# Kernel tuning notes

Hardware: AMD Instinct MI355X
Metric: run time of the kernel (lower is better)

The kernel has to match this reference:

```python
import jax, jax.numpy as jnp
import numpy as np

B, S, D, H, MLP = 8, 1024, 768, 12, 3072
HD = D // H
EPS = 1e-5


def setup_inputs() -> dict:
    key = jax.random.key(0)
    ks = jax.random.split(key, 5)
    sd = lambda fan_in: 1.0 / np.sqrt(fan_in)
    return {
        "x": jax.random.normal(ks[0], (B, S, D), jnp.float32),
        "w_qkv": jax.random.normal(ks[1], (D, 3 * D), jnp.float32) * sd(D),
        "w_out": jax.random.normal(ks[2], (D, D), jnp.float32) * sd(D),
        "b_out": jnp.zeros((D,), jnp.float32),
        "w1": jax.random.normal(ks[3], (D, MLP), jnp.float32) * sd(D),
        "b1": jnp.zeros((MLP,), jnp.float32),
        "w2": jax.random.normal(ks[4], (MLP, D), jnp.float32) * sd(MLP),
        "b2": jnp.zeros((D,), jnp.float32),
    }


def _instance_norm(x):
    # torch InstanceNorm2d on a 3D [B,S,D] tensor treats it as unbatched (C,H,W):
    # normalize over (S, D) per batch element, biased var, eps=1e-5, no affine.
    mu = jnp.mean(x, axis=(1, 2), keepdims=True)
    var = jnp.mean(jnp.square(x - mu), axis=(1, 2), keepdims=True)
    return (x - mu) * jax.lax.rsqrt(var + EPS)


def reference(x, w_qkv, w_out, b_out, w1, b1, w2, b2):
    scale = HD ** -0.5
    # --- self-attention branch ---
    h = _instance_norm(x)
    qkv = (h @ w_qkv).reshape(B, S, 3, H, HD)          # (qkv, heads, head_dim) split
    qkv = qkv.transpose(2, 0, 3, 1, 4)                  # [3, B, H, S, HD]
    q, k, v = qkv[0], qkv[1], qkv[2]
    att = jax.nn.softmax(jnp.einsum('bhxd,bhyd->bhxy', q, k) * scale, axis=-1)
    o = jnp.einsum('bhxy,bhyd->bhxd', att, v)           # [B, H, S, HD]
    o = o.transpose(0, 2, 1, 3).reshape(B, S, D)        # b h l d -> b l (h d)
    x = x + (o @ w_out + b_out)
    # --- MLP branch (exact erf GELU, as nn.GELU default) ---
    h2 = _instance_norm(x)
    m = jax.nn.gelu(h2 @ w1 + b1, approximate=False) @ w2 + b2
    return x + m
```

## Files before the change

kernel.cpp:

```cpp
#include <hip/hip_runtime.h>
#include <hip/hip_bf16.h>

typedef __hip_bfloat16 bf16;
typedef __attribute__((ext_vector_type(8))) short short8;
typedef __attribute__((ext_vector_type(4))) float f32x4;

#define B_   8
#define S_   1024
#define D_   768
#define H_   12
#define HD_  64
#define MLP_ 3072
#define SD_  (S_ * D_)

#define QSCALE 0.18033688011112042f

__device__ __forceinline__ float b2f(short h) {
  union { unsigned u; float f; } w;
  w.u = ((unsigned)(unsigned short)h) << 16;
  return w.f;
}

__device__ __forceinline__ float fast_exp2(float x) {
  float r;
  asm("v_exp_f32 %0, %1" : "=v"(r) : "v"(x));
  return r;
}

__device__ __forceinline__ bf16 fastbf(float f) {
  union { float f; unsigned u; } w; w.f = f;
  unsigned r = (w.u + 0x7FFF + ((w.u >> 16) & 1)) >> 16;
  union { unsigned short s; bf16 b; } o; o.s = (unsigned short)r;
  return o.b;
}

__device__ __forceinline__ float roundbf(float f) {
  union { float f; unsigned u; } w; w.f = f;
  w.u = ((w.u + 0x7FFF + ((w.u >> 16) & 1)) >> 16) << 16;
  return w.f;
}

__device__ __forceinline__ void gl2lds16(const bf16* g, bf16* l) {
  __builtin_amdgcn_global_load_lds(
      (const __attribute__((address_space(1))) unsigned*)(const void*)g,
      (__attribute__((address_space(3))) unsigned*)(void*)l, 16, 0, 0);
}

__global__ __launch_bounds__(256) void transpose_stats(
    const float* __restrict__ w_qkv, const float* __restrict__ w_out,
    const float* __restrict__ w1, const float* __restrict__ w2,
    bf16* __restrict__ t_qkv, bf16* __restrict__ t_out,
    bf16* __restrict__ t1, bf16* __restrict__ t2,
    const float* __restrict__ x, bf16* __restrict__ xb,
    float* __restrict__ redp, float* __restrict__ cs1, float* __restrict__ csq,
    float* __restrict__ red2) {
  const int t = blockIdx.x;
  if (t == 0 && threadIdx.x < 16) red2[threadIdx.x] = 0.f;

  if (t >= 7680) {
    const float* wsrc; float* cdst; int C, n0;
    if (t < 7692) { wsrc = w1;    cdst = cs1; C = 3072; n0 = (t - 7680) * 256; }
    else          { wsrc = w_qkv; cdst = csq; C = 2304; n0 = (t - 7692) * 256; }
    const int n = n0 + threadIdx.x;
    float s = 0.f;
#pragma unroll 8
    for (int k = 0; k < 768; ++k)
      s += roundbf(wsrc[(long)k * C + n]);
    cdst[n] = s;
    return;
  }

  if (t >= 6912) {
    const int bi = t - 6912;
    const long off = (long)bi * 8192;
    float s = 0.f, s2 = 0.f;
#pragma unroll
    for (int it = 0; it < 4; ++it) {
      const long i = off + ((long)threadIdx.x + it * 256) * 8;
      float4 v0 = *(const float4*)(x + i);
      float4 v1 = *(const float4*)(x + i + 4);
      s += v0.x + v0.y + v0.z + v0.w + v1.x + v1.y + v1.z + v1.w;
      s2 += v0.x * v0.x + v0.y * v0.y + v0.z * v0.z + v0.w * v0.w +
            v1.x * v1.x + v1.y * v1.y + v1.z * v1.z + v1.w * v1.w;
      __align__(16) bf16 tmp[8];
      tmp[0] = __float2bfloat16(v0.x); tmp[1] = __float2bfloat16(v0.y);
      tmp[2] = __float2bfloat16(v0.z); tmp[3] = __float2bfloat16(v0.w);
      tmp[4] = __float2bfloat16(v1.x); tmp[5] = __float2bfloat16(v1.y);
      tmp[6] = __float2bfloat16(v1.z); tmp[7] = __float2bfloat16(v1.w);
      *(short8*)(xb + i) = *(const short8*)tmp;
    }
#pragma unroll
    for (int o = 1; o < 64; o <<= 1) { s += __shfl_xor(s, o, 64); s2 += __shfl_xor(s2, o, 64); }
    __shared__ float sh[8];
    const int wave = threadIdx.x >> 6, lane = threadIdx.x & 63;
    if (lane == 0) { sh[wave * 2] = s; sh[wave * 2 + 1] = s2; }
    __syncthreads();
    if (threadIdx.x == 0) {
      redp[bi * 2]     = sh[0] + sh[2] + sh[4] + sh[6];
      redp[bi * 2 + 1] = sh[1] + sh[3] + sh[5] + sh[7];
    }
    return;
  }

  const float* in; bf16* out; int R, C, idx;
  if (t < 1728)      { in = w_qkv; out = t_qkv; R = 768;  C = 2304; idx = t; }
  else if (t < 2304) { in = w_out; out = t_out; R = 768;  C = 768;  idx = t - 1728; }
  else if (t < 4608) { in = w1;    out = t1;    R = 768;  C = 3072; idx = t - 2304; }
  else               { in = w2;    out = t2;    R = 3072; C = 768;  idx = t - 4608; }
  const int nbx = C >> 5;
  const int bx = (idx % nbx) * 32, by = (idx / nbx) * 32;
  __shared__ float tt[32][33];
  const int tx = threadIdx.x & 31, ty = threadIdx.x >> 5;
#pragma unroll
  for (int rr = 0; rr < 32; rr += 8)
    tt[ty + rr][tx] = in[(long)(by + ty + rr) * C + bx + tx];
  __syncthreads();
#pragma unroll
  for (int rr = 0; rr < 32; rr += 8)
    out[(long)(bx + ty + rr) * R + by + tx] = __float2bfloat16(tt[tx][ty + rr]);
}

template <int EPI, bool STATS>
__global__ __launch_bounds__(256) void gemm_k(
    const bf16* __restrict__ A, const bf16* __restrict__ Bt,
    int M, int N, int K,
    const float* __restrict__ biasf, const float* __restrict__ resf,
    const float* __restrict__ cs, const float* __restrict__ stat_in,
    float* __restrict__ outf,
    bf16* __restrict__ outb0, bf16* __restrict__ outb1, bf16* __restrict__ outb2,
    float* __restrict__ statp) {
  __shared__ __align__(16) bf16 As[128 * 64];
  __shared__ __align__(16) bf16 Bs[128 * 64];
  __shared__ float sred[8];
  const int tid = threadIdx.x;
  const int bm = blockIdx.x * 128, bn = blockIdx.y * 128;
  const int wave = tid >> 6, lane = tid & 63;
  const int quad = lane >> 4, l16 = lane & 15;
  const int wm = (wave >> 1) * 64, wn = (wave & 1) * 64;
  const int swz = l16 & 7;

  f32x4 acc[4][4];
#pragma unroll
  for (int i = 0; i < 4; ++i)
#pragma unroll
    for (int j = 0; j < 4; ++j) acc[i][j] = (f32x4){0.f, 0.f, 0.f, 0.f};

  const int srow = tid >> 3;
  const int sgc = (tid & 7) ^ (srow & 7);
  const bf16* Ab = A + (long)(bm + srow) * K + sgc * 8;
  const bf16* Bb = Bt + (long)(bn + srow) * K + sgc * 8;

  auto stage = [&](int k0) {
#pragma unroll
    for (int s = 0; s < 4; ++s)
      gl2lds16(Ab + (long)(s * 32) * K + k0, &As[0] + s * 2048 + tid * 8);
#pragma unroll
    for (int s = 0; s < 4; ++s)
      gl2lds16(Bb + (long)(s * 32) * K + k0, &Bs[0] + s * 2048 + tid * 8);
  };

  stage(0);
  const int nk = K >> 6;
  for (int kt = 0; kt < nk; ++kt) {
    __syncthreads();
    short8 a[2][4], b[2][4];
#pragma unroll
    for (int kk = 0; kk < 2; ++kk) {
      const int co = ((kk * 4 + quad) ^ swz) * 8;
#pragma unroll
      for (int i = 0; i < 4; ++i)
        a[kk][i] = *(const short8*)(&As[0] + (wm + i * 16 + l16) * 64 + co);
#pragma unroll
      for (int j = 0; j < 4; ++j)
        b[kk][j] = *(const short8*)(&Bs[0] + (wn + j * 16 + l16) * 64 + co);
    }
    __syncthreads();
    if (kt + 1 < nk) stage((kt + 1) * 64);
#pragma unroll
    for (int kk = 0; kk < 2; ++kk)
#pragma unroll
      for (int i = 0; i < 4; ++i)
#pragma unroll
        for (int j = 0; j < 4; ++j)
          acc[i][j] = __builtin_amdgcn_mfma_f32_16x16x32_bf16(a[kk][i], b[kk][j], acc[i][j], 0, 0, 0);
  }

  const int m0 = bm + wm + quad * 4;
  const int n0 = bn + wn + l16;
  const int batch = bm >> 10;
  float mu = 0.f, rs = 0.f;
  if (EPI == 0) {
    float s1 = 0.f, s2v = 0.f;
    const float* pp = stat_in + batch * 192;
#pragma unroll 8
    for (int k = 0; k < 96; ++k) { s1 += pp[k * 2]; s2v += pp[k * 2 + 1]; }
    mu = s1 * (1.0f / SD_);
    rs = rsqrtf(s2v * (1.0f / SD_) - mu * mu + 1e-5f);
  } else if (EPI == 2) {
    const float s1 = stat_in[batch * 2], s2v = stat_in[batch * 2 + 1];
    mu = s1 * (1.0f / SD_);
    rs = rsqrtf(s2v * (1.0f / SD_) - mu * mu + 1e-5f);
  }
  float ts = 0.f, ts2 = 0.f;
#pragma unroll
  for (int i = 0; i < 4; ++i) {
#pragma unroll
    for (int j = 0; j < 4; ++j) {
      const int n = n0 + j * 16;
#pragma unroll
      for (int r = 0; r < 4; ++r) {
        const int m = m0 + i * 16 + r;
        float v = acc[i][j][r];
        if (EPI == 0) {
          v = rs * (v - mu * cs[n]);
          const int t = n / D_;
          const int rr2 = n - t * D_;
          const int hh = rr2 >> 6, dd = rr2 & 63;
          const int bb = m >> 10, ss = m & 1023;
          const long hoff = (long)(bb * H_ + hh);
          if (t == 0)      outb0[(hoff * S_ + ss) * HD_ + dd] = __float2bfloat16(v * QSCALE);
          else if (t == 1) outb1[(hoff * S_ + ss) * HD_ + dd] = __float2bfloat16(v);
          else             outb2[(hoff * HD_ + dd) * S_ + ss] = __float2bfloat16(v);
        } else if (EPI == 1) {
          v += biasf[n] + resf[(long)m * N + n];
          outf[(long)m * N + n] = v;
          outb0[(long)m * N + n] = __float2bfloat16(v);
          if (STATS) { ts += v; ts2 += v * v; }
        } else if (EPI == 2) {
          v = rs * (v - mu * cs[n]) + biasf[n];
          float u = v * v;
          float y = v * (1.0f + 0.044715f * u) * 0.7978845608028654f;
          float z = fast_exp2(y * -2.885390081777927f);
          v = v * __builtin_amdgcn_rcpf(1.0f + z);
          outb0[(long)m * N + n] = __float2bfloat16(v);
        } else {
          v += biasf[n] + resf[(long)m * N + n];
          outf[(long)m * N + n] = v;
        }
      }
    }
  }
  if (STATS) {
#pragma unroll
    for (int o = 1; o < 64; o <<= 1) { ts += __shfl_xor(ts, o, 64); ts2 += __shfl_xor(ts2, o, 64); }
    if (lane == 0) { sred[wave * 2] = ts; sred[wave * 2 + 1] = ts2; }
    __syncthreads();
    if (tid == 0) {
      atomicAdd(&statp[batch * 2], sred[0] + sred[2] + sred[4] + sred[6]);
      atomicAdd(&statp[batch * 2 + 1], sred[1] + sred[3] + sred[5] + sred[7]);
    }
  }
}

__global__ __launch_bounds__(512) void attn64(const bf16* __restrict__ q,
                                              const bf16* __restrict__ k,
                                              const bf16* __restrict__ vt,
                                              bf16* __restrict__ o) {
  __shared__ __align__(16) bf16 Ks[2][64 * 64];
  __shared__ __align__(16) bf16 Vs[2][64 * 64];
  const int bh = blockIdx.x, qt = blockIdx.y;
  const int tid = threadIdx.x, wave = tid >> 6, lane = tid & 63;
  const int quad = lane >> 4, l16 = lane & 15;
  const int sw = (l16 & 7) ^ ((l16 >> 3) & 1);
  const long base = (long)bh * (S_ * HD_);
  const bf16* kg = k + base;
  const bf16* vg = vt + base;

  const int srow = tid >> 3;
  const int scg = (tid & 7) ^ (srow & 7) ^ ((srow >> 3) & 1);

  short8 aq[2];
#pragma unroll
  for (int kk = 0; kk < 2; ++kk)
    aq[kk] = *(const short8*)(q + base + (long)(qt * 128 + wave * 16 + l16) * HD_ +
                              kk * 32 + quad * 8);

  gl2lds16(kg + (long)srow * HD_ + scg * 8, &Ks[0][0] + tid * 8);
  gl2lds16(vg + (long)srow * S_ + scg * 8, &Vs[0][0] + tid * 8);

  const bf16* kp = kg + (long)(64 + srow) * HD_ + scg * 8;
  const bf16* vp = vg + (long)srow * S_ + 64 + scg * 8;

  f32x4 oacc[4];
#pragma unroll
  for (int j = 0; j < 4; ++j) oacc[j] = (f32x4){0.f, 0.f, 0.f, 0.f};
  float lp = 0.f;

  const int vh = (quad & 1) * 4;

#define ATTN_STEP(CUR, DOPREF)                                                 \
  {                                                                            \
    __syncthreads();                                                           \
    if (DOPREF) {               \
      gl2lds16(kp, &Ks[(CUR) ^ 1][0] + tid * 8);                               \
      gl2lds16(vp, &Vs[(CUR) ^ 1][0] + tid * 8);                               \
      kp += 64 * HD_;                                                          \
      vp += 64;                                                                \
    }                                                                          \
    f32x4 s[4];                                                                \
    _Pragma("unroll")                                                          \
    for (int i = 0; i < 4; ++i) s[i] = (f32x4){0.f, 0.f, 0.f, 0.f};            \
    __builtin_amdgcn_s_setprio(1);                                             \
    _Pragma("unroll")                                                          \
    for (int kk = 0; kk < 2; ++kk) {                                           \
      _Pragma("unroll")                                                        \
      for (int i = 0; i < 4; ++i) {                                            \
        short8 ak = *(const short8*)(&Ks[CUR][0] + (i * 16 + l16) * 64 +       \
                                     (((kk * 4 + quad) ^ sw) * 8));            \
        s[i] = __builtin_amdgcn_mfma_f32_16x16x32_bf16(ak, aq[kk], s[i], 0, 0, 0); \
      }                                                                        \
    }                                                                          \
    __builtin_amdgcn_s_setprio(0);                                             \
    float pe[4][4];                                                            \
    _Pragma("unroll")                                                          \
    for (int i = 0; i < 4; ++i) {                                              \
      _Pragma("unroll")                                                        \
      for (int r = 0; r < 4; ++r) { pe[i][r] = fast_exp2(s[i][r]); lp += pe[i][r]; } \
    }                                                                          \
    union { short8 v; bf16 b[8]; } af[2];                                      \
    _Pragma("unroll")                                                          \
    for (int r = 0; r < 4; ++r) {                                              \
      af[0].b[r]     = fastbf(pe[0][r]);                                       \
      af[0].b[4 + r] = fastbf(pe[1][r]);                                       \
      af[1].b[r]     = fastbf(pe[2][r]);                                       \
      af[1].b[4 + r] = fastbf(pe[3][r]);                                       \
    }                                                                          \
    __builtin_amdgcn_s_setprio(1);                                             \
    _Pragma("unroll")                                                          \
    for (int kk = 0; kk < 2; ++kk) {                                           \
      const int g0 = ((4 * kk + (quad >> 1)) ^ sw) * 8 + vh;                   \
      const int g1 = ((4 * kk + 2 + (quad >> 1)) ^ sw) * 8 + vh;               \
      _Pragma("unroll")                                                        \
      for (int dj = 0; dj < 4; ++dj) {                                         \
        const bf16* vrow = &Vs[CUR][0] + (dj * 16 + l16) * 64;                 \
        union { short8 v; uint2 u[2]; } bv;                                    \
        bv.u[0] = *(const uint2*)(vrow + g0);                                  \
        bv.u[1] = *(const uint2*)(vrow + g1);                                  \
        oacc[dj] = __builtin_amdgcn_mfma_f32_16x16x32_bf16(af[kk].v, bv.v, oacc[dj], 0, 0, 0); \
      }                                                                        \
    }                                                                          \
    __builtin_amdgcn_s_setprio(0);                                             \
  }

  for (int c = 0; c < 16; c += 2) {
    ATTN_STEP(0, true)
    ATTN_STEP(1, (c < 14))
  }
#undef ATTN_STEP

  float lt = lp;
  lt += __shfl_xor(lt, 16, 64);
  lt += __shfl_xor(lt, 32, 64);

  const int b = bh / H_, hh = bh - b * H_;
#pragma unroll
  for (int r = 0; r < 4; ++r) {
    const float inv = 1.0f / __shfl(lt, quad * 4 + r, 64);
    const int sg = qt * 128 + wave * 16 + quad * 4 + r;
    const long rowoff = ((long)b * S_ + sg) * D_ + hh * HD_;
#pragma unroll
    for (int dj = 0; dj < 4; ++dj)
      o[rowoff + dj * 16 + l16] = __float2bfloat16(oacc[dj][r] * inv);
  }
}

extern "C" void kernel_launch(void* const* d_in, const int* in_sizes, int n_in,
                              void* d_out, int out_size, void* d_ws, size_t ws_size,
                              hipStream_t stream) {
  const float* x     = (const float*)d_in[0];
  const float* w_qkv = (const float*)d_in[1];
  const float* w_out = (const float*)d_in[2];
  const float* b_out = (const float*)d_in[3];
  const float* w1    = (const float*)d_in[4];
  const float* b1    = (const float*)d_in[5];
  const float* w2    = (const float*)d_in[6];
  const float* b2    = (const float*)d_in[7];
  float* out = (float*)d_out;

  bf16* wt_qkv = (bf16*)d_ws;
  bf16* wt_out = wt_qkv + 2304 * 768;
  bf16* wt1    = wt_out + 768 * 768;
  bf16* wt2    = wt1 + 3072 * 768;
  bf16* qb     = wt2 + 768 * 3072;
  bf16* kb     = qb + 6291456;
  bf16* vtb    = kb + 6291456;
  bf16* ob     = vtb + 6291456;
  float* x1f   = (float*)(ob + 6291456);
  bf16* hb     = (bf16*)(x1f + 6291456);
  float* redp  = (float*)(hb + 6291456);
  float* red_x = redp + 1536;
  float* red2  = red_x + 16;
  float* cs1   = red2 + 16;
  float* csq   = cs1 + 3072;
  bf16* gb     = qb;
  bf16* xb     = hb;
  bf16* x1b    = hb;

  transpose_stats<<<7701, 256, 0, stream>>>(w_qkv, w_out, w1, w2,
                                            wt_qkv, wt_out, wt1, wt2,
                                            x, xb, redp, cs1, csq, red2);

  gemm_k<0, false><<<dim3(64, 18), 256, 0, stream>>>(
      xb, wt_qkv, 8192, 2304, 768, nullptr, nullptr, csq, redp,
      nullptr, qb, kb, vtb, nullptr);
  attn64<<<dim3(B_ * H_, 8), 512, 0, stream>>>(qb, kb, vtb, ob);

  gemm_k<1, true><<<dim3(64, 6), 256, 0, stream>>>(
      ob, wt_out, 8192, 768, 768, b_out, x, nullptr, nullptr,
      x1f, x1b, nullptr, nullptr, red2);

  gemm_k<2, false><<<dim3(64, 24), 256, 0, stream>>>(
      x1b, wt1, 8192, 3072, 768, b1, nullptr, cs1, red2,
      nullptr, gb, nullptr, nullptr, nullptr);

  gemm_k<3, false><<<dim3(64, 6), 256, 0, stream>>>(
      gb, wt2, 8192, 768, 3072, b2, x1f, nullptr, nullptr,
      out, nullptr, nullptr, nullptr, nullptr);
}
```

Measured before the change: 352.5 us.

## Use atomic per-batch stats for input norm and halve attention block size

The input instance-norm partial sums are now atomically accumulated into per-batch totals, which a memset zeroes first, so the QKV GEMM no longer re-sums 96 partials per block. The attention kernel moves from 512-thread blocks of 128 queries to 256-thread blocks of 64 queries, doubling the grid. Each thread now issues two K/V LDS loads per tile, and the s_setprio hints around the MFMA sections are dropped. This adds a memset launch and atomic contention, and it doubles the total K/V reloads in attention.

```diff
diff --git a/kernel.cpp b/kernel.cpp
--- a/kernel.cpp
+++ b/kernel.cpp
@@ -46,16 +46,15 @@
       (__attribute__((address_space(3))) unsigned*)(void*)l, 16, 0, 0);
 }
 
-__global__ __launch_bounds__(256) void transpose_stats(
+__global__ __launch_bounds__(256) void prep_all(
     const float* __restrict__ w_qkv, const float* __restrict__ w_out,
     const float* __restrict__ w1, const float* __restrict__ w2,
     bf16* __restrict__ t_qkv, bf16* __restrict__ t_out,
     bf16* __restrict__ t1, bf16* __restrict__ t2,
     const float* __restrict__ x, bf16* __restrict__ xb,
-    float* __restrict__ redp, float* __restrict__ cs1, float* __restrict__ csq,
-    float* __restrict__ red2) {
+    float* __restrict__ red_x, float* __restrict__ cs1,
+    float* __restrict__ csq) {
   const int t = blockIdx.x;
-  if (t == 0 && threadIdx.x < 16) red2[threadIdx.x] = 0.f;
 
   if (t >= 7680) {
     const float* wsrc; float* cdst; int C, n0;
@@ -96,8 +95,9 @@
     if (lane == 0) { sh[wave * 2] = s; sh[wave * 2 + 1] = s2; }
     __syncthreads();
     if (threadIdx.x == 0) {
-      redp[bi * 2]     = sh[0] + sh[2] + sh[4] + sh[6];
-      redp[bi * 2 + 1] = sh[1] + sh[3] + sh[5] + sh[7];
+      const int bb = bi / 96;
+      atomicAdd(&red_x[bb * 2],     sh[0] + sh[2] + sh[4] + sh[6]);
+      atomicAdd(&red_x[bb * 2 + 1], sh[1] + sh[3] + sh[5] + sh[7]);
     }
     return;
   }
@@ -189,14 +189,7 @@
   const int n0 = bn + wn + l16;
   const int batch = bm >> 10;
   float mu = 0.f, rs = 0.f;
-  if (EPI == 0) {
-    float s1 = 0.f, s2v = 0.f;
-    const float* pp = stat_in + batch * 192;
-#pragma unroll 8
-    for (int k = 0; k < 96; ++k) { s1 += pp[k * 2]; s2v += pp[k * 2 + 1]; }
-    mu = s1 * (1.0f / SD_);
-    rs = rsqrtf(s2v * (1.0f / SD_) - mu * mu + 1e-5f);
-  } else if (EPI == 2) {
+  if (EPI == 0 || EPI == 2) {
     const float s1 = stat_in[batch * 2], s2v = stat_in[batch * 2 + 1];
     mu = s1 * (1.0f / SD_);
     rs = rsqrtf(s2v * (1.0f / SD_) - mu * mu + 1e-5f);
@@ -252,7 +245,7 @@
   }
 }
 
-__global__ __launch_bounds__(512) void attn64(const bf16* __restrict__ q,
+__global__ __launch_bounds__(256) void attn64(const bf16* __restrict__ q,
                                               const bf16* __restrict__ k,
                                               const bf16* __restrict__ vt,
                                               bf16* __restrict__ o) {
@@ -272,11 +265,13 @@
   short8 aq[2];
 #pragma unroll
   for (int kk = 0; kk < 2; ++kk)
-    aq[kk] = *(const short8*)(q + base + (long)(qt * 128 + wave * 16 + l16) * HD_ +
+    aq[kk] = *(const short8*)(q + base + (long)(qt * 64 + wave * 16 + l16) * HD_ +
                               kk * 32 + quad * 8);
 
   gl2lds16(kg + (long)srow * HD_ + scg * 8, &Ks[0][0] + tid * 8);
+  gl2lds16(kg + (long)(32 + srow) * HD_ + scg * 8, &Ks[0][0] + 2048 + tid * 8);
   gl2lds16(vg + (long)srow * S_ + scg * 8, &Vs[0][0] + tid * 8);
+  gl2lds16(vg + (long)(32 + srow) * S_ + scg * 8, &Vs[0][0] + 2048 + tid * 8);
 
   const bf16* kp = kg + (long)(64 + srow) * HD_ + scg * 8;
   const bf16* vp = vg + (long)srow * S_ + 64 + scg * 8;
@@ -293,14 +288,15 @@
     __syncthreads();                                                           \
     if (DOPREF) {               \
       gl2lds16(kp, &Ks[(CUR) ^ 1][0] + tid * 8);                               \
+      gl2lds16(kp + 32 * HD_, &Ks[(CUR) ^ 1][0] + 2048 + tid * 8);             \
       gl2lds16(vp, &Vs[(CUR) ^ 1][0] + tid * 8);                               \
+      gl2lds16(vp + 32 * (long)S_, &Vs[(CUR) ^ 1][0] + 2048 + tid * 8);        \
       kp += 64 * HD_;                                                          \
       vp += 64;                                                                \
     }                                                                          \
     f32x4 s[4];                                                                \
     _Pragma("unroll")                                                          \
     for (int i = 0; i < 4; ++i) s[i] = (f32x4){0.f, 0.f, 0.f, 0.f};            \
-    __builtin_amdgcn_s_setprio(1);                                             \
     _Pragma("unroll")                                                          \
     for (int kk = 0; kk < 2; ++kk) {                                           \
       _Pragma("unroll")                                                        \
@@ -310,7 +306,6 @@
         s[i] = __builtin_amdgcn_mfma_f32_16x16x32_bf16(ak, aq[kk], s[i], 0, 0, 0); \
       }                                                                        \
     }                                                                          \
-    __builtin_amdgcn_s_setprio(0);                                             \
     float pe[4][4];                                                            \
     _Pragma("unroll")                                                          \
     for (int i = 0; i < 4; ++i) {                                              \
@@ -325,7 +320,6 @@
       af[1].b[r]     = fastbf(pe[2][r]);                                       \
       af[1].b[4 + r] = fastbf(pe[3][r]);                                       \
     }                                                                          \
-    __builtin_amdgcn_s_setprio(1);                                             \
     _Pragma("unroll")                                                          \
     for (int kk = 0; kk < 2; ++kk) {                                           \
       const int g0 = ((4 * kk + (quad >> 1)) ^ sw) * 8 + vh;                   \
@@ -339,7 +333,6 @@
         oacc[dj] = __builtin_amdgcn_mfma_f32_16x16x32_bf16(af[kk].v, bv.v, oacc[dj], 0, 0, 0); \
       }                                                                        \
     }                                                                          \
-    __builtin_amdgcn_s_setprio(0);                                             \
   }
 
   for (int c = 0; c < 16; c += 2) {
@@ -356,7 +349,7 @@
 #pragma unroll
   for (int r = 0; r < 4; ++r) {
     const float inv = 1.0f / __shfl(lt, quad * 4 + r, 64);
-    const int sg = qt * 128 + wave * 16 + quad * 4 + r;
+    const int sg = qt * 64 + wave * 16 + quad * 4 + r;
     const long rowoff = ((long)b * S_ + sg) * D_ + hh * HD_;
 #pragma unroll
     for (int dj = 0; dj < 4; ++dj)
@@ -396,14 +389,16 @@
   bf16* xb     = hb;
   bf16* x1b    = hb;
 
-  transpose_stats<<<7701, 256, 0, stream>>>(w_qkv, w_out, w1, w2,
-                                            wt_qkv, wt_out, wt1, wt2,
-                                            x, xb, redp, cs1, csq, red2);
+  hipMemsetAsync(red_x, 0, 32 * sizeof(float), stream);
+
+  prep_all<<<7701, 256, 0, stream>>>(w_qkv, w_out, w1, w2,
+                                     wt_qkv, wt_out, wt1, wt2,
+                                     x, xb, red_x, cs1, csq);
 
   gemm_k<0, false><<<dim3(64, 18), 256, 0, stream>>>(
-      xb, wt_qkv, 8192, 2304, 768, nullptr, nullptr, csq, redp,
+      xb, wt_qkv, 8192, 2304, 768, nullptr, nullptr, csq, red_x,
       nullptr, qb, kb, vtb, nullptr);
-  attn64<<<dim3(B_ * H_, 8), 512, 0, stream>>>(qb, kb, vtb, ob);
+  attn64<<<dim3(B_ * H_, 16), 256, 0, stream>>>(qb, kb, vtb, ob);
 
   gemm_k<1, true><<<dim3(64, 6), 256, 0, stream>>>(
       ob, wt_out, 8192, 768, 768, b_out, x, nullptr, nullptr,
```

Result: slower. 370.1 us (+5.0%).
